# Optimization experiments

Hardware: AMD Instinct MI355X
Metric: run time of the kernel (lower is better)

## Reference

```python
import jax, jax.numpy as jnp
import numpy as np

TWO_PI = 2.0 * np.pi
EPS = 1e-12  # torch F.normalize eps


def setup_inputs() -> dict:
    key = jax.random.key(0)
    ks = jax.random.split(key, 12)
    B, NS, G = 16, 128, 20000
    P, S, E, T = 200, 128, 128, 50
    return {
        "x_genes": jax.random.normal(ks[0], (B, NS, G), jnp.float32),
        "tissue_idx": jax.random.randint(ks[1], (B, NS), 0, T, jnp.int32),
        "pathway_idx": jax.random.randint(ks[2], (P, S), 0, G, jnp.int32),
        "W_proj": jax.random.normal(ks[3], (P, E, S), jnp.float32) * (1.0 / np.sqrt(S)),
        "b_proj": jax.random.normal(ks[4], (P, E), jnp.float32) * 0.02,
        "tissue_table": jax.random.normal(ks[5], (T, E), jnp.float32),
        "W1": jax.random.normal(ks[6], (E, 32), jnp.float32) * (1.0 / np.sqrt(E)),
        "b1": jax.random.normal(ks[7], (32,), jnp.float32) * 0.02,
        "W2": jax.random.normal(ks[8], (32, 2), jnp.float32) * (1.0 / np.sqrt(32)),
        "b2": jax.random.normal(ks[9], (2,), jnp.float32) * 0.02,
        "Wdec": jax.random.normal(ks[10], (2, G), jnp.float32) * (1.0 / np.sqrt(2.0)),
        "bdec": jax.random.normal(ks[11], (G,), jnp.float32) * 0.02,
    }


def _l2norm(v):
    n = jnp.sqrt(jnp.sum(v * v, axis=-1, keepdims=True))
    return v / jnp.maximum(n, EPS)


def reference(x_genes, tissue_idx, pathway_idx, W_proj, b_proj, tissue_table,
              W1, b1, W2, b2, Wdec, bdec):
    B, NS, G = x_genes.shape
    x = x_genes.reshape(-1, G)            # [N, G], N = B*NS
    t = tissue_idx.reshape(-1)            # [N]

    # Pathway tokenizer: gather gene subsets + per-pathway linear (grouped GEMM)
    xg = x[:, pathway_idx]                # [N, P, S]
    H = jax.nn.relu(jnp.einsum('nps,pes->npe', xg, W_proj) + b_proj)  # [N, P, E]

    # Single-query attention with tissue embedding as query
    Q = tissue_table[t]                   # [N, E]
    scale = 1.0 / np.sqrt(H.shape[-1])
    scores = jnp.einsum('ne,npe->np', Q, H) * scale   # [N, P]
    attn = jax.nn.softmax(scores, axis=-1)
    context = jnp.einsum('np,npe->ne', attn, H)       # [N, E]

    # to_latent MLP (dropout=0 / eval)
    h = jax.nn.relu(context @ W1 + b1)
    pc = h @ W2 + b2                      # [N, 2]
    pcn = _l2norm(pc)
    ang = jnp.remainder(jnp.arctan2(pcn[:, 1], pcn[:, 0]) + TWO_PI, TWO_PI)

    # decode + normalize
    rec = _l2norm(pcn @ Wdec + bdec)      # [N, G]

    return (pcn.reshape(B, NS, 2), ang.reshape(B, NS), rec.reshape(B, NS, G))
```

## Files before the change

### kernel.cpp

```cpp
#include <hip/hip_runtime.h>
#include <cmath>

#define GG 20000
#define NN 2048
#define PP 200
#define SS 128
#define EE 128
#define TN 128
#define TPP 8
#define NOCT 25

typedef __bf16 bf16x8 __attribute__((ext_vector_type(8)));
typedef float f32x16 __attribute__((ext_vector_type(16)));
typedef unsigned short u16x8 __attribute__((ext_vector_type(8)));

__device__ __align__(16) unsigned g_xTi[(size_t)GG * NN];
__device__ __align__(16) unsigned short g_Wsw[(size_t)PP * 32768];
__device__ float g_ctxp[(size_t)NN * NOCT * EE];
__device__ float g_mT[NOCT * NN];
__device__ float g_lT[NOCT * NN];
__device__ float g_statsp[6][64];

__device__ __forceinline__ unsigned short f2bf(float f) {
  unsigned u = __builtin_bit_cast(unsigned, f);
  return (unsigned short)((u + 0x7FFFu + ((u >> 16) & 1u)) >> 16);
}
__device__ __forceinline__ float bf2f(unsigned short h) {
  return __builtin_bit_cast(float, (unsigned)h << 16);
}
__device__ __forceinline__ unsigned packhl(float f) {
  unsigned short h = f2bf(f);
  unsigned short l = f2bf(f - bf2f(h));
  return (unsigned)h | ((unsigned)l << 16);
}

__global__ __launch_bounds__(256) void transpose_convert_kernel(
    const float* __restrict__ x)
{
  __shared__ unsigned tile[128 * 129];
  const int g0 = blockIdx.x * 128;
  const int n0 = blockIdx.y * 128;
  const int t = threadIdx.x;

  {
    const int gq = t & 31, nr = t >> 5;
    const int g = g0 + gq * 4;
    #pragma unroll
    for (int k = 0; k < 16; ++k) {
      int nl = nr + 8 * k;
      unsigned v0 = 0, v1 = 0, v2 = 0, v3 = 0;
      if (g + 3 < GG) {
        float4 v = *(const float4*)&x[(size_t)(n0 + nl) * GG + g];
        v0 = packhl(v.x); v1 = packhl(v.y); v2 = packhl(v.z); v3 = packhl(v.w);
      }
      unsigned* row = &tile[nl * 129 + gq * 4];
      row[0] = v0; row[1] = v1; row[2] = v2; row[3] = v3;
    }
  }
  __syncthreads();
  {
    const int nq = t & 31, gr = t >> 5;
    #pragma unroll
    for (int k = 0; k < 16; ++k) {
      int gl = gr + 8 * k;
      int g = g0 + gl;
      if (g < GG) {
        uint4 o;
        o.x = tile[(nq * 4 + 0) * 129 + gl];
        o.y = tile[(nq * 4 + 1) * 129 + gl];
        o.z = tile[(nq * 4 + 2) * 129 + gl];
        o.w = tile[(nq * 4 + 3) * 129 + gl];
        *(uint4*)&g_xTi[(size_t)g * NN + n0 + nq * 4] = o;
      }
    }
  }
}

__global__ __launch_bounds__(256) void wconvert_kernel(const float* __restrict__ Wp)
{
  unsigned v = blockIdx.x * 256 + threadIdx.x;
  const int si = v & 7;
  const int slp = (v >> 3) & 7;
  const int e = (v >> 6) & 127;
  const int ch = (v >> 13) & 1;
  const int p = v >> 14;
  const int slot = slp ^ (e & 7);
  const int s = ch * 64 + slot * 8 + si;
  float f = Wp[((size_t)p * EE + e) * SS + s];
  unsigned short h = f2bf(f);
  unsigned short l = f2bf(f - bf2f(h));
  size_t base = (size_t)(p * 2 + ch) * 16384 + e * 64 + slp * 8 + si;
  g_Wsw[base] = h;
  g_Wsw[base + 8192] = l;
}

__global__ __launch_bounds__(256) void wdec_stats_partial(
    const float* __restrict__ Wdec, const float* __restrict__ bdec)
{
  __shared__ float red[6][4];
  const int b = blockIdx.x;
  const int start = b * 313;
  const int end = (start + 313 < GG) ? start + 313 : GG;
  float s00 = 0, s11 = 0, s01 = 0, t0 = 0, t1 = 0, sbb = 0;
  for (int g = start + threadIdx.x; g < end; g += 256) {
    float w0 = Wdec[g], w1 = Wdec[GG + g], bb = bdec[g];
    s00 += w0 * w0; s11 += w1 * w1; s01 += w0 * w1;
    t0 += w0 * bb;  t1 += w1 * bb;  sbb += bb * bb;
  }
  #pragma unroll
  for (int off = 32; off >= 1; off >>= 1) {
    s00 += __shfl_xor(s00, off); s11 += __shfl_xor(s11, off);
    s01 += __shfl_xor(s01, off); t0 += __shfl_xor(t0, off);
    t1 += __shfl_xor(t1, off);   sbb += __shfl_xor(sbb, off);
  }
  const int w = threadIdx.x >> 6;
  if ((threadIdx.x & 63) == 0) {
    red[0][w] = s00; red[1][w] = s11; red[2][w] = s01;
    red[3][w] = t0;  red[4][w] = t1;  red[5][w] = sbb;
  }
  __syncthreads();
  if (threadIdx.x < 6)
    g_statsp[threadIdx.x][b] = red[threadIdx.x][0] + red[threadIdx.x][1] +
                               red[threadIdx.x][2] + red[threadIdx.x][3];
}

__device__ __forceinline__ void load16(unsigned* xr, const int* sidx_lds,
                                       int sbase, int kh, int ncol) {
  #pragma unroll
  for (int ks2 = 0; ks2 < 2; ++ks2)
    #pragma unroll
    for (int j = 0; j < 8; ++j) {
      int s = (sbase + ks2) * 16 + kh * 8 + j;
      xr[ks2 * 8 + j] = g_xTi[(size_t)sidx_lds[s] * NN + ncol];
    }
}

__device__ __forceinline__ void compute2ks(const unsigned short* wb,
                                           const unsigned* xr, f32x16 (&acc)[4],
                                           int klbase, int nl, int kh) {
  #pragma unroll
  for (int ks2 = 0; ks2 < 2; ++ks2) {
    const int ksl = klbase + ks2;
    const unsigned short* wAh = wb;
    const unsigned short* wAl = wb + 8192;
    u16x8 bhu, blu;
    #pragma unroll
    for (int j = 0; j < 8; ++j) {
      unsigned v = xr[ks2 * 8 + j];
      bhu[j] = (unsigned short)(v & 0xffffu);
      blu[j] = (unsigned short)(v >> 16);
    }
    bf16x8 bh = __builtin_bit_cast(bf16x8, bhu);
    bf16x8 bl = __builtin_bit_cast(bf16x8, blu);
    #pragma unroll
    for (int et = 0; et < 4; ++et) {
      const int e = et * 32 + nl;
      const int slp = (ksl * 2 + kh) ^ (e & 7);
      bf16x8 ah = __builtin_bit_cast(bf16x8, *(const uint4*)(wAh + e * 64 + slp * 8));
      bf16x8 al = __builtin_bit_cast(bf16x8, *(const uint4*)(wAl + e * 64 + slp * 8));
      acc[et] = __builtin_amdgcn_mfma_f32_32x32x16_bf16(ah, bh, acc[et], 0, 0, 0);
      acc[et] = __builtin_amdgcn_mfma_f32_32x32x16_bf16(ah, bl, acc[et], 0, 0, 0);
      acc[et] = __builtin_amdgcn_mfma_f32_32x32x16_bf16(al, bh, acc[et], 0, 0, 0);
    }
  }
}

__device__ __forceinline__ void pathway_body(
    int p, unsigned short* wbuf, int* sidx, float* sbp,
    const int* __restrict__ pidx, const float* __restrict__ bp,
    const float* __restrict__ tt, int tid_n,
    int t, int w, int ln, int nl, int kh, int ncol,
    f32x16 (&h)[4], float& s_out)
{
  #pragma unroll
  for (int et = 0; et < 4; ++et)
    #pragma unroll
    for (int r = 0; r < 16; ++r) h[et][r] = 0.f;

  #pragma unroll
  for (int ch = 0; ch < 2; ++ch) {
    __syncthreads();
    if (ch == 0) {
      if (t < 128) sidx[t] = pidx[p * SS + t];
      else         sbp[t - 128] = bp[p * EE + (t - 128)];
    }
    {
      const unsigned short* src = g_Wsw + (size_t)(p * 2 + ch) * 16384 + w * 4096 + ln * 8;
      unsigned short* dst = wbuf + w * 4096;
      #pragma unroll
      for (int j = 0; j < 8; ++j) {
        __builtin_amdgcn_global_load_lds(
            (const __attribute__((address_space(1))) unsigned int*)(src + j * 512),
            (__attribute__((address_space(3))) unsigned int*)(dst + j * 512), 16, 0, 0);
      }
    }
    __syncthreads();

    unsigned xa[16], xb[16];
    load16(xa, sidx, ch * 4 + 0, kh, ncol);
    load16(xb, sidx, ch * 4 + 2, kh, ncol);
    compute2ks(wbuf, xa, h, 0, nl, kh);
    compute2ks(wbuf, xb, h, 2, nl, kh);
  }

  const float4* qp = (const float4*)(tt + (size_t)tid_n * EE);
  float scr = 0.f;
  #pragma unroll
  for (int et = 0; et < 4; ++et)
    #pragma unroll
    for (int rq = 0; rq < 4; ++rq) {
      int e0 = et * 32 + rq * 8 + kh * 4;
      float4 q4 = qp[e0 >> 2];
      float4 b4 = *(const float4*)&sbp[e0];
      float h0 = fmaxf(h[et][rq * 4 + 0] + b4.x, 0.f);
      float h1 = fmaxf(h[et][rq * 4 + 1] + b4.y, 0.f);
      float h2 = fmaxf(h[et][rq * 4 + 2] + b4.z, 0.f);
      float h3 = fmaxf(h[et][rq * 4 + 3] + b4.w, 0.f);
      h[et][rq * 4 + 0] = h0; h[et][rq * 4 + 1] = h1;
      h[et][rq * 4 + 2] = h2; h[et][rq * 4 + 3] = h3;
      scr += h0 * q4.x + h1 * q4.y + h2 * q4.z + h3 * q4.w;
    }
  scr += __shfl_xor(scr, 32);
  s_out = scr * 0.08838834764831845f;
}

__global__ __launch_bounds__(256, 2) void proj_mfma_kernel(
    const int* __restrict__ tidx, const int* __restrict__ pidx,
    const float* __restrict__ bp, const float* __restrict__ tt)
{
  __shared__ __align__(16) unsigned short wbuf[16384];
  __shared__ int sidx[SS];
  __shared__ float sbp[EE];

  const int t = threadIdx.x;
  const int w = t >> 6;
  const int ln = t & 63;
  const int nl = ln & 31;
  const int kh = ln >> 5;
  const int n0 = blockIdx.x * TN;
  const int oct = blockIdx.y;
  const int ncol = n0 + w * 32 + nl;
  const int tid_n = tidx[ncol];

  f32x16 ctx[4];
  #pragma unroll
  for (int et = 0; et < 4; ++et)
    #pragma unroll
    for (int r = 0; r < 16; ++r) ctx[et][r] = 0.f;
  float m_r = -1e30f, l_r = 0.f;

  f32x16 h[4];
  float s;
  for (int pp = 0; pp < TPP; ++pp) {
    pathway_body(oct * TPP + pp, wbuf, sidx, sbp, pidx, bp, tt, tid_n,
                 t, w, ln, nl, kh, ncol, h, s);
    const float mn = fmaxf(m_r, s);
    const float f = expf(m_r - mn);
    const float wg = expf(s - mn);
    l_r = l_r * f + wg;
    m_r = mn;
    #pragma unroll
    for (int et = 0; et < 4; ++et)
      #pragma unroll
      for (int r = 0; r < 16; ++r)
        ctx[et][r] = ctx[et][r] * f + wg * h[et][r];
  }

  __syncthreads();
  float* tbase = (float*)wbuf;
  #pragma unroll
  for (int ph = 0; ph < 2; ++ph) {
    if ((w >> 1) == ph) {
      float* tb = tbase + (w & 1) * 4096;
      #pragma unroll
      for (int et = 0; et < 4; ++et)
        #pragma unroll
        for (int rq = 0; rq < 4; ++rq) {
          int slot = et * 8 + rq * 2 + kh;
          float4 v = make_float4(ctx[et][rq * 4 + 0], ctx[et][rq * 4 + 1],
                                 ctx[et][rq * 4 + 2], ctx[et][rq * 4 + 3]);
          *(float4*)&tb[nl * 128 + ((slot ^ nl) << 2)] = v;
        }
      const int rrow = ln >> 1, eh = (ln & 1) * 16;
      const int nn = n0 + w * 32 + rrow;
      float* dst = g_ctxp + ((size_t)nn * NOCT + oct) * EE + eh * 4;
      const float* srcrow = tb + rrow * 128;
      #pragma unroll
      for (int k = 0; k < 16; ++k) {
        int slot = eh + k;
        *(float4*)&dst[k * 4] = *(const float4*)&srcrow[(slot ^ rrow) << 2];
      }
    }
    __syncthreads();
  }
  if (ln < 32) {
    g_mT[oct * NN + ncol] = m_r;
    g_lT[oct * NN + ncol] = l_r;
  }
}

__global__ __launch_bounds__(256) void combine_rec_kernel(
    const float* __restrict__ W1, const float* __restrict__ b1,
    const float* __restrict__ W2, const float* __restrict__ b2,
    const float* __restrict__ Wdec, const float* __restrict__ bdec,
    float* __restrict__ out)
{
  const int n = blockIdx.x;
  const int t = threadIdx.x;
  __shared__ float ws[NOCT];
  __shared__ float ctx2[2][EE];
  __shared__ float r1[4], r2[4];
  __shared__ float hsh[32];
  __shared__ float qsh[3];
  __shared__ float stats_s[6];

  if (t >= 192 && t < 198) {
    float v = 0.f;
    #pragma unroll 8
    for (int j = 0; j < 64; ++j) v += g_statsp[t - 192][j];
    stats_s[t - 192] = v;
  }

  float mv = (t < NOCT) ? g_mT[t * NN + n] : -1e30f;
  float lv = (t < NOCT) ? g_lT[t * NN + n] : 0.f;
  float M = mv;
  #pragma unroll
  for (int off = 32; off >= 1; off >>= 1) M = fmaxf(M, __shfl_xor(M, off));
  if ((t & 63) == 0) r1[t >> 6] = M;
  __syncthreads();
  M = fmaxf(fmaxf(r1[0], r1[1]), fmaxf(r1[2], r1[3]));
  float wv = (t < NOCT) ? expf(mv - M) : 0.f;
  if (t < NOCT) ws[t] = wv;
  float Lp = wv * lv;
  #pragma unroll
  for (int off = 32; off >= 1; off >>= 1) Lp += __shfl_xor(Lp, off);
  if ((t & 63) == 0) r2[t >> 6] = Lp;
  __syncthreads();
  const float L = r2[0] + r2[1] + r2[2] + r2[3];

  {
    const int e = t & 127, hf = t >> 7;
    const int sA = hf ? 13 : 0, sB = hf ? NOCT : 13;
    const float* base = g_ctxp + ((size_t)n * NOCT + sA) * EE + e;
    float c = 0.f;
    for (int s = sA; s < sB; ++s) c += ws[s] * base[(size_t)(s - sA) * EE];
    ctx2[hf][e] = c;
  }
  __syncthreads();
  const float invL = 1.f / L;
  if (t < 32) {
    float h = 0.f;
    for (int e = 0; e < EE; ++e) h += (ctx2[0][e] + ctx2[1][e]) * W1[e * 32 + t];
    hsh[t] = fmaxf(h * invL + b1[t], 0.f);
  }
  __syncthreads();
  if (t == 0) {
    float p0 = b2[0], p1 = b2[1];
    #pragma unroll
    for (int k = 0; k < 32; ++k) { p0 += hsh[k] * W2[k * 2]; p1 += hsh[k] * W2[k * 2 + 1]; }
    float invp = 1.f / fmaxf(sqrtf(p0 * p0 + p1 * p1), 1e-12f);
    float q0 = p0 * invp, q1 = p1 * invp;
    const float PI2 = 6.2831853071795864769f;
    float ang = atan2f(q1, q0) + PI2;
    if (ang >= PI2) ang -= PI2;
    out[n * 2 + 0] = q0;
    out[n * 2 + 1] = q1;
    out[2 * NN + n] = ang;
    float n2 = q0 * q0 * stats_s[0] + q1 * q1 * stats_s[1] +
               2.f * q0 * q1 * stats_s[2] +
               2.f * q0 * stats_s[3] + 2.f * q1 * stats_s[4] + stats_s[5];
    qsh[0] = q0;
    qsh[1] = q1;
    qsh[2] = 1.f / fmaxf(sqrtf(n2), 1e-12f);
  }
  __syncthreads();
  const float q0 = qsh[0], q1 = qsh[1], inv = qsh[2];

  float* orec = out + 3 * NN + (size_t)n * GG;
  for (int i = t; i < GG / 4; i += 256) {
    float4 w0 = *(const float4*)&Wdec[i * 4];
    float4 w1 = *(const float4*)&Wdec[GG + i * 4];
    float4 b4 = *(const float4*)&bdec[i * 4];
    float4 o;
    o.x = (q0 * w0.x + q1 * w1.x + b4.x) * inv;
    o.y = (q0 * w0.y + q1 * w1.y + b4.y) * inv;
    o.z = (q0 * w0.z + q1 * w1.z + b4.z) * inv;
    o.w = (q0 * w0.w + q1 * w1.w + b4.w) * inv;
    *(float4*)&orec[i * 4] = o;
  }
}

extern "C" void kernel_launch(void* const* d_in, const int* in_sizes, int n_in,
                              void* d_out, int out_size, void* d_ws, size_t ws_size,
                              hipStream_t stream) {
  (void)in_sizes; (void)n_in; (void)out_size; (void)d_ws; (void)ws_size;
  const float* x    = (const float*)d_in[0];
  const int*   tidx = (const int*)  d_in[1];
  const int*   pidx = (const int*)  d_in[2];
  const float* Wp   = (const float*)d_in[3];
  const float* bp   = (const float*)d_in[4];
  const float* tt   = (const float*)d_in[5];
  const float* W1   = (const float*)d_in[6];
  const float* b1   = (const float*)d_in[7];
  const float* W2   = (const float*)d_in[8];
  const float* b2   = (const float*)d_in[9];
  const float* Wdec = (const float*)d_in[10];
  const float* bdec = (const float*)d_in[11];
  float* out = (float*)d_out;

  dim3 gridT((GG + 127) / 128, NN / 128, 1);
  transpose_convert_kernel<<<gridT, 256, 0, stream>>>(x);
  wconvert_kernel<<<(PP * 16384) / 256, 256, 0, stream>>>(Wp);
  wdec_stats_partial<<<64, 256, 0, stream>>>(Wdec, bdec);

  dim3 gridA(NN / TN, NOCT, 1);
  proj_mfma_kernel<<<gridA, 256, 0, stream>>>(tidx, pidx, bp, tt);

  combine_rec_kernel<<<NN, 256, 0, stream>>>(W1, b1, W2, b2, Wdec, bdec, out);
}
```

Baseline: 290.7 us.

## Switch projection GEMM to 16x16x32 MFMA with smaller column tiles

Measured after the change: 294.5 us. No clear change (+1.3%).

```diff
diff --git a/kernel.cpp b/kernel.cpp
--- a/kernel.cpp
+++ b/kernel.cpp
@@ -6,12 +6,12 @@
 #define PP 200
 #define SS 128
 #define EE 128
-#define TN 128
+#define TN 64
 #define TPP 8
 #define NOCT 25
 
 typedef __bf16 bf16x8 __attribute__((ext_vector_type(8)));
-typedef float f32x16 __attribute__((ext_vector_type(16)));
+typedef float f32x4 __attribute__((ext_vector_type(4)));
 typedef unsigned short u16x8 __attribute__((ext_vector_type(8)));
 
 __device__ __align__(16) unsigned g_xTi[(size_t)GG * NN];
@@ -124,107 +124,7 @@
                                red[threadIdx.x][2] + red[threadIdx.x][3];
 }
 
-__device__ __forceinline__ void load16(unsigned* xr, const int* sidx_lds,
-                                       int sbase, int kh, int ncol) {
-  #pragma unroll
-  for (int ks2 = 0; ks2 < 2; ++ks2)
-    #pragma unroll
-    for (int j = 0; j < 8; ++j) {
-      int s = (sbase + ks2) * 16 + kh * 8 + j;
-      xr[ks2 * 8 + j] = g_xTi[(size_t)sidx_lds[s] * NN + ncol];
-    }
-}
-
-__device__ __forceinline__ void compute2ks(const unsigned short* wb,
-                                           const unsigned* xr, f32x16 (&acc)[4],
-                                           int klbase, int nl, int kh) {
-  #pragma unroll
-  for (int ks2 = 0; ks2 < 2; ++ks2) {
-    const int ksl = klbase + ks2;
-    const unsigned short* wAh = wb;
-    const unsigned short* wAl = wb + 8192;
-    u16x8 bhu, blu;
-    #pragma unroll
-    for (int j = 0; j < 8; ++j) {
-      unsigned v = xr[ks2 * 8 + j];
-      bhu[j] = (unsigned short)(v & 0xffffu);
-      blu[j] = (unsigned short)(v >> 16);
-    }
-    bf16x8 bh = __builtin_bit_cast(bf16x8, bhu);
-    bf16x8 bl = __builtin_bit_cast(bf16x8, blu);
-    #pragma unroll
-    for (int et = 0; et < 4; ++et) {
-      const int e = et * 32 + nl;
-      const int slp = (ksl * 2 + kh) ^ (e & 7);
-      bf16x8 ah = __builtin_bit_cast(bf16x8, *(const uint4*)(wAh + e * 64 + slp * 8));
-      bf16x8 al = __builtin_bit_cast(bf16x8, *(const uint4*)(wAl + e * 64 + slp * 8));
-      acc[et] = __builtin_amdgcn_mfma_f32_32x32x16_bf16(ah, bh, acc[et], 0, 0, 0);
-      acc[et] = __builtin_amdgcn_mfma_f32_32x32x16_bf16(ah, bl, acc[et], 0, 0, 0);
-      acc[et] = __builtin_amdgcn_mfma_f32_32x32x16_bf16(al, bh, acc[et], 0, 0, 0);
-    }
-  }
-}
-
-__device__ __forceinline__ void pathway_body(
-    int p, unsigned short* wbuf, int* sidx, float* sbp,
-    const int* __restrict__ pidx, const float* __restrict__ bp,
-    const float* __restrict__ tt, int tid_n,
-    int t, int w, int ln, int nl, int kh, int ncol,
-    f32x16 (&h)[4], float& s_out)
-{
-  #pragma unroll
-  for (int et = 0; et < 4; ++et)
-    #pragma unroll
-    for (int r = 0; r < 16; ++r) h[et][r] = 0.f;
-
-  #pragma unroll
-  for (int ch = 0; ch < 2; ++ch) {
-    __syncthreads();
-    if (ch == 0) {
-      if (t < 128) sidx[t] = pidx[p * SS + t];
-      else         sbp[t - 128] = bp[p * EE + (t - 128)];
-    }
-    {
-      const unsigned short* src = g_Wsw + (size_t)(p * 2 + ch) * 16384 + w * 4096 + ln * 8;
-      unsigned short* dst = wbuf + w * 4096;
-      #pragma unroll
-      for (int j = 0; j < 8; ++j) {
-        __builtin_amdgcn_global_load_lds(
-            (const __attribute__((address_space(1))) unsigned int*)(src + j * 512),
-            (__attribute__((address_space(3))) unsigned int*)(dst + j * 512), 16, 0, 0);
-      }
-    }
-    __syncthreads();
-
-    unsigned xa[16], xb[16];
-    load16(xa, sidx, ch * 4 + 0, kh, ncol);
-    load16(xb, sidx, ch * 4 + 2, kh, ncol);
-    compute2ks(wbuf, xa, h, 0, nl, kh);
-    compute2ks(wbuf, xb, h, 2, nl, kh);
-  }
-
-  const float4* qp = (const float4*)(tt + (size_t)tid_n * EE);
-  float scr = 0.f;
-  #pragma unroll
-  for (int et = 0; et < 4; ++et)
-    #pragma unroll
-    for (int rq = 0; rq < 4; ++rq) {
-      int e0 = et * 32 + rq * 8 + kh * 4;
-      float4 q4 = qp[e0 >> 2];
-      float4 b4 = *(const float4*)&sbp[e0];
-      float h0 = fmaxf(h[et][rq * 4 + 0] + b4.x, 0.f);
-      float h1 = fmaxf(h[et][rq * 4 + 1] + b4.y, 0.f);
-      float h2 = fmaxf(h[et][rq * 4 + 2] + b4.z, 0.f);
-      float h3 = fmaxf(h[et][rq * 4 + 3] + b4.w, 0.f);
-      h[et][rq * 4 + 0] = h0; h[et][rq * 4 + 1] = h1;
-      h[et][rq * 4 + 2] = h2; h[et][rq * 4 + 3] = h3;
-      scr += h0 * q4.x + h1 * q4.y + h2 * q4.z + h3 * q4.w;
-    }
-  scr += __shfl_xor(scr, 32);
-  s_out = scr * 0.08838834764831845f;
-}
-
-__global__ __launch_bounds__(256, 2) void proj_mfma_kernel(
+__global__ __launch_bounds__(256, 3) void proj_mfma_kernel(
     const int* __restrict__ tidx, const int* __restrict__ pidx,
     const float* __restrict__ bp, const float* __restrict__ tt)
 {
@@ -235,65 +135,107 @@
   const int t = threadIdx.x;
   const int w = t >> 6;
   const int ln = t & 63;
-  const int nl = ln & 31;
-  const int kh = ln >> 5;
+  const int c = ln & 15;
+  const int q = ln >> 4;
   const int n0 = blockIdx.x * TN;
   const int oct = blockIdx.y;
-  const int ncol = n0 + w * 32 + nl;
+  const int ncol = n0 + w * 16 + c;
   const int tid_n = tidx[ncol];
 
-  f32x16 ctx[4];
-  #pragma unroll
-  for (int et = 0; et < 4; ++et)
-    #pragma unroll
-    for (int r = 0; r < 16; ++r) ctx[et][r] = 0.f;
+  f32x4 ctx[8];
+  #pragma unroll
+  for (int t8 = 0; t8 < 8; ++t8)
+    #pragma unroll
+    for (int r = 0; r < 4; ++r) ctx[t8][r] = 0.f;
   float m_r = -1e30f, l_r = 0.f;
 
-  f32x16 h[4];
-  float s;
   for (int pp = 0; pp < TPP; ++pp) {
-    pathway_body(oct * TPP + pp, wbuf, sidx, sbp, pidx, bp, tt, tid_n,
-                 t, w, ln, nl, kh, ncol, h, s);
-    const float mn = fmaxf(m_r, s);
+    const int p = oct * TPP + pp;
+    f32x4 h[8];
+    #pragma unroll
+    for (int t8 = 0; t8 < 8; ++t8)
+      #pragma unroll
+      for (int r = 0; r < 4; ++r) h[t8][r] = 0.f;
+
+    #pragma unroll
+    for (int ch = 0; ch < 2; ++ch) {
+      __syncthreads();
+      if (ch == 0) {
+        if (t < 128) sidx[t] = pidx[p * SS + t];
+        else         sbp[t - 128] = bp[p * EE + (t - 128)];
+      }
+      {
+        const unsigned short* src = g_Wsw + (size_t)(p * 2 + ch) * 16384 + w * 4096 + ln * 8;
+        unsigned short* dst = wbuf + w * 4096;
+        #pragma unroll
+        for (int j = 0; j < 8; ++j) {
+          __builtin_amdgcn_global_load_lds(
+              (const __attribute__((address_space(1))) unsigned int*)(src + j * 512),
+              (__attribute__((address_space(3))) unsigned int*)(dst + j * 512), 16, 0, 0);
+        }
+      }
+      __syncthreads();
+
+      #pragma unroll
+      for (int ks = 0; ks < 2; ++ks) {
+        const int sb = ch * 64 + ks * 32 + q * 8;
+        u16x8 bhu, blu;
+        #pragma unroll
+        for (int j = 0; j < 8; ++j) {
+          unsigned v = g_xTi[(size_t)sidx[sb + j] * NN + ncol];
+          bhu[j] = (unsigned short)(v & 0xffffu);
+          blu[j] = (unsigned short)(v >> 16);
+        }
+        bf16x8 bh = __builtin_bit_cast(bf16x8, bhu);
+        bf16x8 bl = __builtin_bit_cast(bf16x8, blu);
+        const int slp = (ks * 4 + q) ^ (c & 7);
+        #pragma unroll
+        for (int t8 = 0; t8 < 8; ++t8) {
+          const int e = t8 * 16 + c;
+          bf16x8 ah = __builtin_bit_cast(bf16x8, *(const uint4*)(wbuf + e * 64 + slp * 8));
+          bf16x8 al = __builtin_bit_cast(bf16x8, *(const uint4*)(wbuf + 8192 + e * 64 + slp * 8));
+          h[t8] = __builtin_amdgcn_mfma_f32_16x16x32_bf16(ah, bh, h[t8], 0, 0, 0);
+          h[t8] = __builtin_amdgcn_mfma_f32_16x16x32_bf16(ah, bl, h[t8], 0, 0, 0);
+          h[t8] = __builtin_amdgcn_mfma_f32_16x16x32_bf16(al, bh, h[t8], 0, 0, 0);
+        }
+      }
+    }
+
+    const float4* qp = (const float4*)(tt + (size_t)tid_n * EE);
+    float scr = 0.f;
+    #pragma unroll
+    for (int t8 = 0; t8 < 8; ++t8) {
+      const int e0 = t8 * 16 + q * 4;
+      float4 q4 = qp[e0 >> 2];
+      float4 b4 = *(const float4*)&sbp[e0];
+      float h0 = fmaxf(h[t8][0] + b4.x, 0.f);
+      float h1 = fmaxf(h[t8][1] + b4.y, 0.f);
+      float h2 = fmaxf(h[t8][2] + b4.z, 0.f);
+      float h3 = fmaxf(h[t8][3] + b4.w, 0.f);
+      h[t8][0] = h0; h[t8][1] = h1; h[t8][2] = h2; h[t8][3] = h3;
+      scr += h0 * q4.x + h1 * q4.y + h2 * q4.z + h3 * q4.w;
+    }
+    scr += __shfl_xor(scr, 16);
+    scr += __shfl_xor(scr, 32);
+    const float s_r = scr * 0.08838834764831845f;
+
+    const float mn = fmaxf(m_r, s_r);
     const float f = expf(m_r - mn);
-    const float wg = expf(s - mn);
+    const float wg = expf(s_r - mn);
     l_r = l_r * f + wg;
     m_r = mn;
     #pragma unroll
-    for (int et = 0; et < 4; ++et)
+    for (int t8 = 0; t8 < 8; ++t8)
       #pragma unroll
-      for (int r = 0; r < 16; ++r)
-        ctx[et][r] = ctx[et][r] * f + wg * h[et][r];
-  }
-
-  __syncthreads();
-  float* tbase = (float*)wbuf;
-  #pragma unroll
-  for (int ph = 0; ph < 2; ++ph) {
-    if ((w >> 1) == ph) {
-      float* tb = tbase + (w & 1) * 4096;
-      #pragma unroll
-      for (int et = 0; et < 4; ++et)
-        #pragma unroll
-        for (int rq = 0; rq < 4; ++rq) {
-          int slot = et * 8 + rq * 2 + kh;
-          float4 v = make_float4(ctx[et][rq * 4 + 0], ctx[et][rq * 4 + 1],
-                                 ctx[et][rq * 4 + 2], ctx[et][rq * 4 + 3]);
-          *(float4*)&tb[nl * 128 + ((slot ^ nl) << 2)] = v;
-        }
-      const int rrow = ln >> 1, eh = (ln & 1) * 16;
-      const int nn = n0 + w * 32 + rrow;
-      float* dst = g_ctxp + ((size_t)nn * NOCT + oct) * EE + eh * 4;
-      const float* srcrow = tb + rrow * 128;
-      #pragma unroll
-      for (int k = 0; k < 16; ++k) {
-        int slot = eh + k;
-        *(float4*)&dst[k * 4] = *(const float4*)&srcrow[(slot ^ rrow) << 2];
-      }
-    }
-    __syncthreads();
-  }
-  if (ln < 32) {
+      for (int r = 0; r < 4; ++r)
+        ctx[t8][r] = ctx[t8][r] * f + wg * h[t8][r];
+  }
+
+  float* dst = g_ctxp + ((size_t)ncol * NOCT + oct) * EE;
+  #pragma unroll
+  for (int t8 = 0; t8 < 8; ++t8)
+    *(f32x4*)&dst[t8 * 16 + q * 4] = ctx[t8];
+  if (ln < 16) {
     g_mT[oct * NN + ncol] = m_r;
     g_lT[oct * NN + ncol] = l_r;
   }
```
